# Optimization experiments

Measured on AMD Instinct MI355X. Metric: run time of the kernel, lower is better.

Reference implementation:

```python
import jax, jax.numpy as jnp
import numpy as np

N_HEADS = 16

def setup_inputs() -> dict:
    key = jax.random.key(0)
    ks = jax.random.split(key, 8)
    B, S, D = 2, 2048, 1024
    s = 0.02
    return {
        "hidden_states": jax.random.normal(ks[0], (B, S, D), jnp.float32),
        "attention_mask": jnp.ones((B, S), jnp.int32),
        "script_types": jax.random.randint(ks[1], (B, S), 0, 4),
        "Wq": jax.random.normal(ks[2], (D, D), jnp.float32) * s,
        "bq": jnp.zeros((D,), jnp.float32),
        "Wk": jax.random.normal(ks[3], (D, D), jnp.float32) * s,
        "bk": jnp.zeros((D,), jnp.float32),
        "Wv": jax.random.normal(ks[4], (D, D), jnp.float32) * s,
        "bv": jnp.zeros((D,), jnp.float32),
        "Wo": jax.random.normal(ks[5], (D, D), jnp.float32) * s,
        "bo": jnp.zeros((D,), jnp.float32),
        "script_w": jnp.ones((4, N_HEADS), jnp.float32),
    }

def _heads(x, H):
    B, S, D = x.shape
    return x.reshape(B, S, H, D // H).transpose(0, 2, 1, 3)  # [B,H,S,hd]

def reference(hidden_states, attention_mask, script_types, Wq, bq, Wk, bk, Wv, bv, Wo, bo, script_w):
    B, S, D = hidden_states.shape
    H = N_HEADS
    hd = D // H
    q = _heads(hidden_states @ Wq + bq, H)
    k = _heads(hidden_states @ Wk + bk, H)
    v = _heads(hidden_states @ Wv + bv, H)
    # script-dependent per-head query scaling: [B,S,H] -> [B,H,S,1]
    sw = script_w[script_types].transpose(0, 2, 1)[..., None]
    q = q * sw
    scores = jnp.einsum("bhqd,bhkd->bhqk", q, k) / jnp.sqrt(jnp.float32(hd))
    mask = attention_mask[:, None, None, :]  # [B,1,1,S]
    scores = jnp.where(mask == 0, -jnp.inf, scores)
    probs = jax.nn.softmax(scores, axis=-1)  # dropout is identity in eval mode
    ctx = jnp.einsum("bhqk,bhkd->bhqd", probs, v)
    ctx = ctx.transpose(0, 2, 1, 3).reshape(B, S, D)
    out = ctx @ Wo + bo
    return out, probs
```

## Files before the change

### kernel.cpp

```cpp
#include <hip/hip_runtime.h>
#include <hip/hip_bf16.h>
#include <cstdint>
#include <cstddef>

typedef __attribute__((ext_vector_type(8))) short short8;
typedef __attribute__((ext_vector_type(4))) float f32x4;

#define MFMA16(a,b,c) __builtin_amdgcn_mfma_f32_16x16x32_bf16((a),(b),(c),0,0,0)
#define NEG_INF (-__builtin_inff())

__device__ __forceinline__ unsigned short f2bf(float f) {
    union { float f; unsigned int u; } a; a.f = f;
    return (unsigned short)((a.u + 0x7FFFu + ((a.u >> 16) & 1u)) >> 16);
}

__device__ __forceinline__ void gload16(const void* g, void* l) {
    __builtin_amdgcn_global_load_lds(
        (const __attribute__((address_space(1))) void*)g,
        (__attribute__((address_space(3))) void*)l, 16, 0, 0);
}

__global__ __launch_bounds__(256) void prep(const float* __restrict__ X,
                                            unsigned short* __restrict__ Xb,
                                            const float* __restrict__ Wq,
                                            const float* __restrict__ Wk,
                                            const float* __restrict__ Wv,
                                            const float* __restrict__ Wo,
                                            unsigned short* __restrict__ WqkvT,
                                            unsigned short* __restrict__ WoT,
                                            const float* __restrict__ bq,
                                            const float* __restrict__ bk,
                                            const float* __restrict__ bv,
                                            float* __restrict__ biasq) {
    const int bid = blockIdx.x;
    const int t = threadIdx.x;
    if (bid < 4096) {
        int i = (bid * 256 + t) * 4;
        float4 v = *(const float4*)(X + i);
        ushort4 o;
        o.x = f2bf(v.x); o.y = f2bf(v.y); o.z = f2bf(v.z); o.w = f2bf(v.w);
        *(ushort4*)(Xb + i) = o;
    } else if (bid < 8192) {
        __shared__ float tile[32][33];
        const int wid = bid - 4096;
        const int which = wid >> 10, t32 = wid & 1023;
        const float* W = (which == 0) ? Wq : (which == 1) ? Wk : (which == 2) ? Wv : Wo;
        unsigned short* WT = (which < 3) ? (WqkvT + which * 1048576) : WoT;
        int tx = t & 31, ty = t >> 5;
        int kb = (t32 & 31) * 32, nb = (t32 >> 5) * 32;
        #pragma unroll
        for (int r = 0; r < 32; r += 8)
            tile[ty + r][tx] = W[(size_t)(kb + ty + r) * 1024 + nb + tx];
        __syncthreads();
        #pragma unroll
        for (int r = 0; r < 32; r += 8) {
            float v = tile[tx][ty + r];
            WT[(size_t)(nb + ty + r) * 1024 + kb + tx] = f2bf(v);
        }
    } else {
        for (int i = t; i < 3072; i += 256) {
            const float* s = (i < 1024) ? bq : (i < 2048) ? bk : bv;
            biasq[i] = s[i & 1023];
        }
    }
}

__global__ __launch_bounds__(256) void transpose_v(const unsigned short* __restrict__ V,
                                                   unsigned short* __restrict__ Vt) {
    __shared__ unsigned short tl[64][65];
    int bh = blockIdx.x >> 5;
    int kt = blockIdx.x & 31;
    int t = threadIdx.x;
    int row = t >> 2, off = (t & 3) * 16;
    const unsigned short* src = V + ((size_t)bh * 2048 + kt * 64 + row) * 64 + off;
    uint4 d0 = *(const uint4*)src;
    uint4 d1 = *(const uint4*)(src + 8);
    unsigned short tmp[16];
    *(uint4*)tmp = d0; *(uint4*)(tmp + 8) = d1;
    #pragma unroll
    for (int e = 0; e < 16; e++) tl[row][off + e] = tmp[e];
    __syncthreads();
    int d = t >> 2, ko = (t & 3) * 16;
    unsigned short o[16];
    #pragma unroll
    for (int e = 0; e < 16; e++) o[e] = tl[ko + e][d];
    unsigned short* dst = Vt + ((size_t)bh * 64 + d) * 2048 + kt * 64 + ko;
    *(uint4*)dst = *(uint4*)o;
    *(uint4*)(dst + 8) = *(uint4*)(o + 8);
}

__global__ __launch_bounds__(256) void gemm_bt(const unsigned short* __restrict__ A,
                                               const unsigned short* __restrict__ BT,
                                               const float* __restrict__ bias,
                                               unsigned short* __restrict__ qkv_out,
                                               float* __restrict__ f32_out,
                                               int mode) {
    __shared__ alignas(16) unsigned short As[4096];
    __shared__ alignas(16) unsigned short Bs[4096];
    const int t = threadIdx.x;
    const int wave = t >> 6, lane = t & 63, quad = lane >> 4, l16 = lane & 15;
    const int m0 = blockIdx.x * 128, n0 = blockIdx.y * 128;
    const int wm = (wave >> 1) * 64, wn = (wave & 1) * 64;
    const int r4 = lane >> 2, c16 = (lane & 3) << 4;
    const char* Ag = (const char*)A + (size_t)(m0 + wave * 32 + r4) * 2048 + c16;
    const char* Bg = (const char*)BT + (size_t)(n0 + wave * 32 + r4) * 2048 + c16;
    char* Al = (char*)As + wave * 2048;
    char* Bl = (char*)Bs + wave * 2048;
    f32x4 acc[4][4] = {};
    for (int k0 = 0; k0 < 1024; k0 += 32) {
        __syncthreads();
        gload16(Ag + k0 * 2, Al);
        gload16(Ag + k0 * 2 + 32768, Al + 1024);
        gload16(Bg + k0 * 2, Bl);
        gload16(Bg + k0 * 2 + 32768, Bl + 1024);
        __syncthreads();
        short8 af[4], bfr[4];
        #pragma unroll
        for (int i = 0; i < 4; i++)
            af[i] = *(const short8*)((const char*)As + (wm + i * 16 + l16) * 64 + (quad << 4));
        #pragma unroll
        for (int j = 0; j < 4; j++)
            bfr[j] = *(const short8*)((const char*)Bs + (wn + j * 16 + l16) * 64 + (quad << 4));
        #pragma unroll
        for (int i = 0; i < 4; i++)
            #pragma unroll
            for (int j = 0; j < 4; j++)
                acc[i][j] = MFMA16(af[i], bfr[j], acc[i][j]);
    }
    #pragma unroll
    for (int i = 0; i < 4; i++) {
        int tokb = m0 + wm + i * 16 + quad * 4;
        #pragma unroll
        for (int j = 0; j < 4; j++) {
            int n = n0 + wn + j * 16 + l16;
            float bv = bias[n];
            #pragma unroll
            for (int r = 0; r < 4; r++) {
                float v = acc[i][j][r] + bv;
                int tok = tokb + r;
                if (mode == 0) {
                    int which = n >> 10, n1 = n & 1023, h = n1 >> 6, d = n1 & 63;
                    int b = tok >> 11, s = tok & 2047;
                    qkv_out[(size_t)which * 4194304 + (((size_t)(b * 16 + h)) * 2048 + s) * 64 + d] = f2bf(v);
                } else {
                    f32_out[(size_t)tok * 1024 + n] = v;
                }
            }
        }
    }
}

__global__ __launch_bounds__(512, 4) void attn(const unsigned short* __restrict__ Q,
                                               const unsigned short* __restrict__ K,
                                               const unsigned short* __restrict__ Vt,
                                               const int* __restrict__ amask,
                                               const int* __restrict__ stypes,
                                               const float* __restrict__ script_w,
                                               float* __restrict__ probs,
                                               unsigned short* __restrict__ ctx) {
    __shared__ alignas(16) unsigned short Ks[2][4096];
    __shared__ alignas(16) unsigned short Vts[2][4096];
    __shared__ alignas(16) unsigned short Ps[8][16][64];
    const int t = threadIdx.x;
    const int wave = t >> 6, lane = t & 63, quad = lane >> 4, l16 = lane & 15;
    const int bid = blockIdx.y * 16 + blockIdx.x;
    const int swz = (bid & 7) * 64 + (bid >> 3);
    const int qt = swz & 15, bh = swz >> 4;
    const int b = bh >> 4, h = bh & 15;
    const int q0 = qt * 128;
    const int qrow = q0 + wave * 16 + l16;
    const int sx16 = (l16 & 7) << 4;

    const int st = stypes[b * 2048 + qrow];
    const float sfac = script_w[st * 16 + h] * 0.125f;

    const size_t qbase = ((size_t)bh * 2048 + qrow) * 64;
    const short8 aQ0 = *(const short8*)(Q + qbase + quad * 8);
    const short8 aQ1 = *(const short8*)(Q + qbase + 32 + quad * 8);

    const char* Kg = (const char*)(K + (size_t)bh * 131072);
    const char* Vg = (const char*)(Vt + (size_t)bh * 131072);
    const int* am = amask + b * 2048;

    const int r8 = lane >> 3;
    const int cx = ((lane & 7) ^ r8) << 4;

#define STAGE_K(kt_, buf_) \
    gload16(Kg + (size_t)(kt_) * 8192 + (wave * 8 + r8) * 128 + cx, \
            (char*)&Ks[buf_][0] + wave * 1024)
#define STAGE_V(kt_, buf_) \
    gload16(Vg + (size_t)(wave * 8 + r8) * 4096 + (kt_) * 128 + cx, \
            (char*)&Vts[buf_][0] + wave * 1024)

    float lsum = 0.f;
    STAGE_K(0, 0);
    __syncthreads();
    {
        int cur = 0;
        for (int kt = 0; kt < 32; kt++) {
            if (kt < 31) STAGE_K(kt + 1, cur ^ 1);
            __builtin_amdgcn_sched_barrier(0);
            f32x4 sc[4] = {};
            const char* kbl = (const char*)&Ks[cur][0];
            #pragma unroll
            for (int j = 0; j < 4; j++) {
                const char* rp = kbl + (j * 16 + l16) * 128;
                short8 bk0 = *(const short8*)(rp + ((quad << 4) ^ sx16));
                short8 bk1 = *(const short8*)(rp + ((64 + (quad << 4)) ^ sx16));
                sc[j] = MFMA16(bk0, aQ0, sc[j]);
                sc[j] = MFMA16(bk1, aQ1, sc[j]);
            }
            #pragma unroll
            for (int j = 0; j < 4; j++) {
                int4 mi = *(const int4*)(am + kt * 64 + j * 16 + quad * 4);
                lsum += __expf(fmaf(sc[j][0], sfac, mi.x ? 0.f : NEG_INF));
                lsum += __expf(fmaf(sc[j][1], sfac, mi.y ? 0.f : NEG_INF));
                lsum += __expf(fmaf(sc[j][2], sfac, mi.z ? 0.f : NEG_INF));
                lsum += __expf(fmaf(sc[j][3], sfac, mi.w ? 0.f : NEG_INF));
            }
            __syncthreads();
            cur ^= 1;
        }
    }
    lsum += __shfl_xor(lsum, 16, 64);
    lsum += __shfl_xor(lsum, 32, 64);
    const float lbias = (lsum > 0.f) ? -__logf(lsum) : NEG_INF;

    f32x4 oacc[4] = {};
    STAGE_K(0, 0);
    STAGE_V(0, 0);
    asm volatile("s_waitcnt vmcnt(0)" ::: "memory");
    __builtin_amdgcn_s_barrier();
    __builtin_amdgcn_sched_barrier(0);
    {
        int cur = 0;
        char* psrow = (char*)&Ps[wave][l16][0];
        for (int kt = 0; kt < 32; kt++) {
            if (kt < 31) { STAGE_K(kt + 1, cur ^ 1); STAGE_V(kt + 1, cur ^ 1); }
            __builtin_amdgcn_sched_barrier(0);
            f32x4 sc[4] = {};
            const char* kbl = (const char*)&Ks[cur][0];
            #pragma unroll
            for (int j = 0; j < 4; j++) {
                const char* rp = kbl + (j * 16 + l16) * 128;
                short8 bk0 = *(const short8*)(rp + ((quad << 4) ^ sx16));
                short8 bk1 = *(const short8*)(rp + ((64 + (quad << 4)) ^ sx16));
                sc[j] = MFMA16(bk0, aQ0, sc[j]);
                sc[j] = MFMA16(bk1, aQ1, sc[j]);
            }
            short8 v0[4], v1[4];
            const char* vbl = (const char*)&Vts[cur][0];
            #pragma unroll
            for (int j2 = 0; j2 < 4; j2++) {
                const char* rp = vbl + (j2 * 16 + l16) * 128;
                v0[j2] = *(const short8*)(rp + ((quad << 4) ^ sx16));
                v1[j2] = *(const short8*)(rp + ((64 + (quad << 4)) ^ sx16));
            }
            const size_t pbase = ((size_t)bh * 2048 + qrow) * 2048 + kt * 64 + quad * 4;
            #pragma unroll
            for (int j = 0; j < 4; j++) {
                int4 mi = *(const int4*)(am + kt * 64 + j * 16 + quad * 4);
                float p0 = __expf(fmaf(sc[j][0], sfac, mi.x ? lbias : NEG_INF));
                float p1 = __expf(fmaf(sc[j][1], sfac, mi.y ? lbias : NEG_INF));
                float p2 = __expf(fmaf(sc[j][2], sfac, mi.z ? lbias : NEG_INF));
                float p3 = __expf(fmaf(sc[j][3], sfac, mi.w ? lbias : NEG_INF));
                float4 pv; pv.x = p0; pv.y = p1; pv.z = p2; pv.w = p3;
                *(float4*)(probs + pbase + j * 16) = pv;
                ushort4 pq; pq.x = f2bf(p0); pq.y = f2bf(p1); pq.z = f2bf(p2); pq.w = f2bf(p3);
                *(ushort4*)(psrow + ((j * 32 + quad * 8) ^ sx16)) = pq;
            }
            asm volatile("s_waitcnt lgkmcnt(0)" ::: "memory");
            __builtin_amdgcn_sched_barrier(0);
            short8 aP0 = *(const short8*)(psrow + ((quad << 4) ^ sx16));
            short8 aP1 = *(const short8*)(psrow + ((64 + (quad << 4)) ^ sx16));
            #pragma unroll
            for (int j2 = 0; j2 < 4; j2++) oacc[j2] = MFMA16(aP0, v0[j2], oacc[j2]);
            #pragma unroll
            for (int j2 = 0; j2 < 4; j2++) oacc[j2] = MFMA16(aP1, v1[j2], oacc[j2]);
            asm volatile("s_waitcnt vmcnt(4)" ::: "memory");
            __builtin_amdgcn_s_barrier();
            __builtin_amdgcn_sched_barrier(0);
            cur ^= 1;
        }
    }
#undef STAGE_K
#undef STAGE_V
    #pragma unroll
    for (int j2 = 0; j2 < 4; j2++)
        #pragma unroll
        for (int r = 0; r < 4; r++) {
            int qr = q0 + wave * 16 + quad * 4 + r;
            ctx[((size_t)b * 2048 + qr) * 1024 + h * 64 + j2 * 16 + l16] = f2bf(oacc[j2][r]);
        }
}

extern "C" void kernel_launch(void* const* d_in, const int* in_sizes, int n_in,
                              void* d_out, int out_size, void* d_ws, size_t ws_size,
                              hipStream_t stream) {
    const float* X    = (const float*)d_in[0];
    const int*  amask = (const int*)d_in[1];
    const int*  stp   = (const int*)d_in[2];
    const float* Wq   = (const float*)d_in[3];
    const float* bq   = (const float*)d_in[4];
    const float* Wk   = (const float*)d_in[5];
    const float* bk   = (const float*)d_in[6];
    const float* Wv   = (const float*)d_in[7];
    const float* bv   = (const float*)d_in[8];
    const float* Wo   = (const float*)d_in[9];
    const float* bo   = (const float*)d_in[10];
    const float* sw   = (const float*)d_in[11];

    float* out   = (float*)d_out;
    float* probs = out + 4194304;

    char* ws = (char*)d_ws;
    unsigned short* Xb    = (unsigned short*)(ws);
    unsigned short* WqkvT = (unsigned short*)(ws + 8388608);
    unsigned short* WoT   = (unsigned short*)(ws + 14680064);
    float*          biasq = (float*)(ws + 16777216);
    unsigned short* Qb    = (unsigned short*)(ws + 16789504);
    unsigned short* Vb    = (unsigned short*)(ws + 33566720);
    unsigned short* Vtb   = (unsigned short*)(ws + 41955328);
    unsigned short* Ctx   = (unsigned short*)(ws + 50343936);
    unsigned short* Kb    = Qb + 4194304;

    prep<<<8193, 256, 0, stream>>>(X, Xb, Wq, Wk, Wv, Wo, WqkvT, WoT, bq, bk, bv, biasq);
    gemm_bt<<<dim3(32, 24), 256, 0, stream>>>(Xb, WqkvT, biasq, Qb, nullptr, 0);
    transpose_v<<<1024, 256, 0, stream>>>(Vb, Vtb);
    attn<<<dim3(16, 32), 512, 0, stream>>>(Qb, Kb, Vtb, amask, stp, sw, probs, Ctx);
    gemm_bt<<<dim3(32, 8), 256, 0, stream>>>(Ctx, WoT, bo, nullptr, out, 1);
}
```

Before: 304.1 us.

## Fuse V transpose into QKV GEMM, retile output GEMM, add setprio and nontemporal probs

The QKV projection epilogue now writes V directly in transposed layout, which removes the separate transpose_v kernel and its round trip through global memory. The output projection gets its own kernel with 64-row tiles, doubling the block count from 256 to 512 so the GPU is better filled. The attention kernel raises wave priority around its MFMA sections and writes the large probs tensor with nontemporal stores so it does not pollute the cache. The transposed V writes are narrow 8-byte strided stores, which may coalesce poorly.

```diff
diff --git a/kernel.cpp b/kernel.cpp
--- a/kernel.cpp
+++ b/kernel.cpp
@@ -65,36 +65,11 @@
     }
 }
 
-__global__ __launch_bounds__(256) void transpose_v(const unsigned short* __restrict__ V,
-                                                   unsigned short* __restrict__ Vt) {
-    __shared__ unsigned short tl[64][65];
-    int bh = blockIdx.x >> 5;
-    int kt = blockIdx.x & 31;
-    int t = threadIdx.x;
-    int row = t >> 2, off = (t & 3) * 16;
-    const unsigned short* src = V + ((size_t)bh * 2048 + kt * 64 + row) * 64 + off;
-    uint4 d0 = *(const uint4*)src;
-    uint4 d1 = *(const uint4*)(src + 8);
-    unsigned short tmp[16];
-    *(uint4*)tmp = d0; *(uint4*)(tmp + 8) = d1;
-    #pragma unroll
-    for (int e = 0; e < 16; e++) tl[row][off + e] = tmp[e];
-    __syncthreads();
-    int d = t >> 2, ko = (t & 3) * 16;
-    unsigned short o[16];
-    #pragma unroll
-    for (int e = 0; e < 16; e++) o[e] = tl[ko + e][d];
-    unsigned short* dst = Vt + ((size_t)bh * 64 + d) * 2048 + kt * 64 + ko;
-    *(uint4*)dst = *(uint4*)o;
-    *(uint4*)(dst + 8) = *(uint4*)(o + 8);
-}
-
-__global__ __launch_bounds__(256) void gemm_bt(const unsigned short* __restrict__ A,
-                                               const unsigned short* __restrict__ BT,
-                                               const float* __restrict__ bias,
-                                               unsigned short* __restrict__ qkv_out,
-                                               float* __restrict__ f32_out,
-                                               int mode) {
+__global__ __launch_bounds__(256) void gemm_qkv(const unsigned short* __restrict__ A,
+                                                const unsigned short* __restrict__ BT,
+                                                const float* __restrict__ bias,
+                                                unsigned short* __restrict__ qk_out,
+                                                unsigned short* __restrict__ vt_out) {
     __shared__ alignas(16) unsigned short As[4096];
     __shared__ alignas(16) unsigned short Bs[4096];
     const int t = threadIdx.x;
@@ -130,22 +105,76 @@
     #pragma unroll
     for (int i = 0; i < 4; i++) {
         int tokb = m0 + wm + i * 16 + quad * 4;
+        int b = tokb >> 11, s = tokb & 2047;
         #pragma unroll
         for (int j = 0; j < 4; j++) {
             int n = n0 + wn + j * 16 + l16;
             float bv = bias[n];
-            #pragma unroll
-            for (int r = 0; r < 4; r++) {
-                float v = acc[i][j][r] + bv;
-                int tok = tokb + r;
-                if (mode == 0) {
-                    int which = n >> 10, n1 = n & 1023, h = n1 >> 6, d = n1 & 63;
-                    int b = tok >> 11, s = tok & 2047;
-                    qkv_out[(size_t)which * 4194304 + (((size_t)(b * 16 + h)) * 2048 + s) * 64 + d] = f2bf(v);
-                } else {
-                    f32_out[(size_t)tok * 1024 + n] = v;
+            int which = n >> 10, n1 = n & 1023, h = n1 >> 6, d = n1 & 63;
+            if (which == 2) {
+                ushort4 pv;
+                pv.x = f2bf(acc[i][j][0] + bv);
+                pv.y = f2bf(acc[i][j][1] + bv);
+                pv.z = f2bf(acc[i][j][2] + bv);
+                pv.w = f2bf(acc[i][j][3] + bv);
+                *(ushort4*)(vt_out + ((size_t)(b * 16 + h) * 64 + d) * 2048 + s) = pv;
+            } else {
+                #pragma unroll
+                for (int r = 0; r < 4; r++) {
+                    float v = acc[i][j][r] + bv;
+                    qk_out[(size_t)which * 4194304 +
+                           (((size_t)(b * 16 + h)) * 2048 + s + r) * 64 + d] = f2bf(v);
                 }
             }
+        }
+    }
+}
+
+__global__ __launch_bounds__(256) void gemm_out(const unsigned short* __restrict__ A,
+                                                const unsigned short* __restrict__ BT,
+                                                const float* __restrict__ bias,
+                                                float* __restrict__ C) {
+    __shared__ alignas(16) unsigned short As[2048];
+    __shared__ alignas(16) unsigned short Bs[4096];
+    const int t = threadIdx.x;
+    const int wave = t >> 6, lane = t & 63, quad = lane >> 4, l16 = lane & 15;
+    const int m0 = blockIdx.x * 64, n0 = blockIdx.y * 128;
+    const int wm = (wave >> 1) * 32, wn = (wave & 1) * 64;
+    const int r4 = lane >> 2, c16 = (lane & 3) << 4;
+    const char* Ag = (const char*)A + (size_t)(m0 + wave * 16 + r4) * 2048 + c16;
+    const char* Bg = (const char*)BT + (size_t)(n0 + wave * 32 + r4) * 2048 + c16;
+    char* Al = (char*)As + wave * 1024;
+    char* Bl = (char*)Bs + wave * 2048;
+    f32x4 acc[2][4] = {};
+    for (int k0 = 0; k0 < 1024; k0 += 32) {
+        __syncthreads();
+        gload16(Ag + k0 * 2, Al);
+        gload16(Bg + k0 * 2, Bl);
+        gload16(Bg + k0 * 2 + 32768, Bl + 1024);
+        __syncthreads();
+        short8 af[2], bfr[4];
+        #pragma unroll
+        for (int i = 0; i < 2; i++)
+            af[i] = *(const short8*)((const char*)As + (wm + i * 16 + l16) * 64 + (quad << 4));
+        #pragma unroll
+        for (int j = 0; j < 4; j++)
+            bfr[j] = *(const short8*)((const char*)Bs + (wn + j * 16 + l16) * 64 + (quad << 4));
+        #pragma unroll
+        for (int i = 0; i < 2; i++)
+            #pragma unroll
+            for (int j = 0; j < 4; j++)
+                acc[i][j] = MFMA16(af[i], bfr[j], acc[i][j]);
+    }
+    #pragma unroll
+    for (int i = 0; i < 2; i++) {
+        int tokb = m0 + wm + i * 16 + quad * 4;
+        #pragma unroll
+        for (int j = 0; j < 4; j++) {
+            int n = n0 + wn + j * 16 + l16;
+            float bv = bias[n];
+            #pragma unroll
+            for (int r = 0; r < 4; r++)
+                C[(size_t)(tokb + r) * 1024 + n] = acc[i][j][r] + bv;
         }
     }
 }
@@ -202,6 +231,7 @@
             __builtin_amdgcn_sched_barrier(0);
             f32x4 sc[4] = {};
             const char* kbl = (const char*)&Ks[cur][0];
+            __builtin_amdgcn_s_setprio(1);
             #pragma unroll
             for (int j = 0; j < 4; j++) {
                 const char* rp = kbl + (j * 16 + l16) * 128;
@@ -210,6 +240,7 @@
                 sc[j] = MFMA16(bk0, aQ0, sc[j]);
                 sc[j] = MFMA16(bk1, aQ1, sc[j]);
             }
+            __builtin_amdgcn_s_setprio(0);
             #pragma unroll
             for (int j = 0; j < 4; j++) {
                 int4 mi = *(const int4*)(am + kt * 64 + j * 16 + quad * 4);
@@ -240,6 +271,7 @@
             __builtin_amdgcn_sched_barrier(0);
             f32x4 sc[4] = {};
             const char* kbl = (const char*)&Ks[cur][0];
+            __builtin_amdgcn_s_setprio(1);
             #pragma unroll
             for (int j = 0; j < 4; j++) {
                 const char* rp = kbl + (j * 16 + l16) * 128;
@@ -248,6 +280,7 @@
                 sc[j] = MFMA16(bk0, aQ0, sc[j]);
                 sc[j] = MFMA16(bk1, aQ1, sc[j]);
             }
+            __builtin_amdgcn_s_setprio(0);
             short8 v0[4], v1[4];
             const char* vbl = (const char*)&Vts[cur][0];
             #pragma unroll
@@ -264,8 +297,8 @@
                 float p1 = __expf(fmaf(sc[j][1], sfac, mi.y ? lbias : NEG_INF));
                 float p2 = __expf(fmaf(sc[j][2], sfac, mi.z ? lbias : NEG_INF));
                 float p3 = __expf(fmaf(sc[j][3], sfac, mi.w ? lbias : NEG_INF));
-                float4 pv; pv.x = p0; pv.y = p1; pv.z = p2; pv.w = p3;
-                *(float4*)(probs + pbase + j * 16) = pv;
+                f32x4 pv; pv[0] = p0; pv[1] = p1; pv[2] = p2; pv[3] = p3;
+                __builtin_nontemporal_store(pv, (f32x4*)(probs + pbase + j * 16));
                 ushort4 pq; pq.x = f2bf(p0); pq.y = f2bf(p1); pq.z = f2bf(p2); pq.w = f2bf(p3);
                 *(ushort4*)(psrow + ((j * 32 + quad * 8) ^ sx16)) = pq;
             }
@@ -273,10 +306,12 @@
             __builtin_amdgcn_sched_barrier(0);
             short8 aP0 = *(const short8*)(psrow + ((quad << 4) ^ sx16));
             short8 aP1 = *(const short8*)(psrow + ((64 + (quad << 4)) ^ sx16));
+            __builtin_amdgcn_s_setprio(1);
             #pragma unroll
             for (int j2 = 0; j2 < 4; j2++) oacc[j2] = MFMA16(aP0, v0[j2], oacc[j2]);
             #pragma unroll
             for (int j2 = 0; j2 < 4; j2++) oacc[j2] = MFMA16(aP1, v1[j2], oacc[j2]);
+            __builtin_amdgcn_s_setprio(0);
             asm volatile("s_waitcnt vmcnt(4)" ::: "memory");
             __builtin_amdgcn_s_barrier();
             __builtin_amdgcn_sched_barrier(0);
@@ -319,14 +354,12 @@
     unsigned short* WoT   = (unsigned short*)(ws + 14680064);
     float*          biasq = (float*)(ws + 16777216);
     unsigned short* Qb    = (unsigned short*)(ws + 16789504);
-    unsigned short* Vb    = (unsigned short*)(ws + 33566720);
     unsigned short* Vtb   = (unsigned short*)(ws + 41955328);
     unsigned short* Ctx   = (unsigned short*)(ws + 50343936);
     unsigned short* Kb    = Qb + 4194304;
 
     prep<<<8193, 256, 0, stream>>>(X, Xb, Wq, Wk, Wv, Wo, WqkvT, WoT, bq, bk, bv, biasq);
-    gemm_bt<<<dim3(32, 24), 256, 0, stream>>>(Xb, WqkvT, biasq, Qb, nullptr, 0);
-    transpose_v<<<1024, 256, 0, stream>>>(Vb, Vtb);
+    gemm_qkv<<<dim3(32, 24), 256, 0, stream>>>(Xb, WqkvT, biasq, Qb, Vtb);
     attn<<<dim3(16, 32), 512, 0, stream>>>(Qb, Kb, Vtb, amask, stp, sw, probs, Ctx);
-    gemm_bt<<<dim3(32, 8), 256, 0, stream>>>(Ctx, WoT, bo, nullptr, out, 1);
-}
+    gemm_out<<<dim3(64, 8), 256, 0, stream>>>(Ctx, WoT, bo, out);
+}
```

After: 296.7 us. -2.4%, faster.
